# Performance work log

Measured on AMD Instinct MI355X. Metric: run time of the kernel, lower is better.

Reference implementation:

```python
import jax, jax.numpy as jnp
import numpy as np

N_NODES = 100_000
N_EDGES = 3_200_000
D = 64           # node and edge feature dim
HID = 36         # hk.nets.MLP hidden size
OUT = 2          # hk.nets.MLP output size
IN_DIM = 3 * D   # nodes + sent_agg + received_agg (globals are None)


def setup_inputs() -> dict:
    key = jax.random.key(0)
    k_n, k_e, k_s, k_r, k_w1, k_w2 = jax.random.split(key, 6)
    nodes = jax.random.normal(k_n, (N_NODES, D), dtype=jnp.float32)
    edges = jax.random.normal(k_e, (N_EDGES, D), dtype=jnp.float32)
    senders = jax.random.randint(k_s, (N_EDGES,), 0, N_NODES, dtype=jnp.int32)
    receivers = jax.random.randint(k_r, (N_EDGES,), 0, N_NODES, dtype=jnp.int32)
    # haiku Linear default init: truncated normal with stddev 1/sqrt(fan_in); plain normal is fine as a stand-in
    W1 = jax.random.normal(k_w1, (IN_DIM, HID), dtype=jnp.float32) / np.sqrt(IN_DIM)
    b1 = jnp.zeros((HID,), dtype=jnp.float32)
    W2 = jax.random.normal(k_w2, (HID, OUT), dtype=jnp.float32) / np.sqrt(HID)
    b2 = jnp.zeros((OUT,), dtype=jnp.float32)
    return {"nodes": nodes, "edges": edges, "senders": senders,
            "receivers": receivers, "W1": W1, "b1": b1, "W2": W2, "b2": b2}


def reference(nodes, edges, senders, receivers, W1, b1, W2, b2):
    # jraph.GraphNetwork node update with update_edge_fn=None, update_global_fn=None:
    #   sent_attributes     = segment_sum(edges, senders,   num_segments=N)
    #   received_attributes = segment_sum(edges, receivers, num_segments=N)
    #   new_nodes = MLP(concat([nodes, sent, received], axis=-1))
    n = nodes.shape[0]
    sent = jax.ops.segment_sum(edges, senders, num_segments=n)       # [N, D]
    recv = jax.ops.segment_sum(edges, receivers, num_segments=n)     # [N, D]
    feats = jnp.concatenate([nodes, sent, recv], axis=-1)            # [N, 3D]
    h = jax.nn.relu(feats @ W1 + b1)                                 # [N, 36]
    new_nodes = h @ W2 + b2                                          # [N, 2] (activate_final=False)
    return new_nodes
```

## Files before the change

### kernel.cpp

```cpp
#include <hip/hip_runtime.h>
#include <hip/hip_bf16.h>

#define D      64
#define HID    36
#define IN_DIM 192
#define NPB    64
#define MAXNB  2048
#define CHUNK  4096
#define SLICE  64

__global__ void zero_ws_kernel(float4* __restrict__ p, long n4) {
    long i = (long)blockIdx.x * blockDim.x + threadIdx.x;
    long stride = (long)gridDim.x * blockDim.x;
    float4 z = make_float4(0.f, 0.f, 0.f, 0.f);
    for (; i < n4; i += stride) p[i] = z;
}

__global__ __launch_bounds__(256) void scatter_kernel(
    const float* __restrict__ edges,
    const int* __restrict__ senders,
    const int* __restrict__ receivers,
    float* __restrict__ sent,
    float* __restrict__ recv,
    long total)
{
    long i = (long)blockIdx.x * blockDim.x + threadIdx.x;
    if (i >= total) return;
    long e = i >> 6;
    int  d = (int)(i & 63);
    float v = edges[i];
    unsafeAtomicAdd(&sent[(long)senders[e] * D + d], v);
    unsafeAtomicAdd(&recv[(long)receivers[e] * D + d], v);
}

__global__ __launch_bounds__(256) void count_kernel(
    const int* __restrict__ senders,
    const int* __restrict__ receivers,
    int* __restrict__ counts,
    int NB, long E, long total_items)
{
    __shared__ int hist[MAXNB];
    for (int b = threadIdx.x; b < NB; b += 256) hist[b] = 0;
    __syncthreads();

    long start = (long)blockIdx.x * CHUNK;
    long end = start + CHUNK; if (end > total_items) end = total_items;
    for (long i = start + threadIdx.x; i < end; i += 256) {
        int node = (i < E) ? senders[i] : receivers[i - E];
        atomicAdd(&hist[node >> 6], 1);
    }
    __syncthreads();
    int* row = counts + (long)blockIdx.x * NB;
    for (int b = threadIdx.x; b < NB; b += 256) row[b] = hist[b];
}

__global__ __launch_bounds__(256) void colscan1_kernel(
    int* __restrict__ counts, int* __restrict__ psum, int NB, int nblocks)
{
    int b = blockIdx.x * 256 + threadIdx.x;
    if (b >= NB) return;
    int s = blockIdx.y;
    int r0 = s * SLICE;
    int r1 = r0 + SLICE; if (r1 > nblocks) r1 = nblocks;
    int run = 0;
    for (int blk = r0; blk < r1; ++blk) {
        long idx = (long)blk * NB + b;
        int c = counts[idx];
        counts[idx] = run;
        run += c;
    }
    psum[(long)s * NB + b] = run;
}

__global__ __launch_bounds__(256) void colscan2_kernel(
    int* __restrict__ psum, int* __restrict__ tot, int NB, int S)
{
    int b = blockIdx.x * 256 + threadIdx.x;
    if (b >= NB) return;
    int run = 0;
    for (int s = 0; s < S; ++s) {
        long i = (long)s * NB + b;
        int v = psum[i];
        psum[i] = run;
        run += v;
    }
    tot[b] = run;
}

__global__ __launch_bounds__(1024) void basescan_kernel(
    const int* __restrict__ tot, int* __restrict__ base, int NB)
{
    __shared__ int sA[2][MAXNB];
    int t = threadIdx.x;
    sA[0][t]        = (t < NB) ? tot[t] : 0;
    sA[0][t + 1024] = (t + 1024 < NB) ? tot[t + 1024] : 0;
    __syncthreads();
    int src = 0;
    for (int off = 1; off < MAXNB; off <<= 1) {
        int dst = src ^ 1;
        int i0 = t, i1 = t + 1024;
        sA[dst][i0] = sA[src][i0] + ((i0 >= off) ? sA[src][i0 - off] : 0);
        sA[dst][i1] = sA[src][i1] + ((i1 >= off) ? sA[src][i1 - off] : 0);
        src = dst;
        __syncthreads();
    }
    if (t < NB)        base[t]        = (t == 0) ? 0 : sA[src][t - 1];
    if (t + 1024 < NB) base[t + 1024] = sA[src][t + 1023];
}

__global__ __launch_bounds__(256) void scatter_ids_kernel(
    const int* __restrict__ senders,
    const int* __restrict__ receivers,
    const int* __restrict__ counts,
    const int* __restrict__ psum,
    const int* __restrict__ base,
    unsigned* __restrict__ pool,
    int NB, long E, long total_items)
{
    __shared__ int cursor[MAXNB];
    const int* row = counts + (long)blockIdx.x * NB;
    const int* srow = psum + (long)(blockIdx.x / SLICE) * NB;
    for (int b = threadIdx.x; b < NB; b += 256)
        cursor[b] = row[b] + srow[b] + base[b];
    __syncthreads();

    long start = (long)blockIdx.x * CHUNK;
    long end = start + CHUNK; if (end > total_items) end = total_items;
    for (long i = start + threadIdx.x; i < end; i += 256) {
        int dir, node; long edge;
        if (i < E) { dir = 0; edge = i;     node = senders[i]; }
        else       { dir = 1; edge = i - E; node = receivers[i - E]; }
        int b = node >> 6;
        int pos = atomicAdd(&cursor[b], 1);
        pool[pos] = ((unsigned)edge << 7) | ((unsigned)dir << 6) | (unsigned)(node & 63);
    }
}

__global__ __launch_bounds__(256) void sort_bucket_kernel(
    const unsigned* __restrict__ pool,
    const int* __restrict__ base,
    const int* __restrict__ tot,
    unsigned* __restrict__ pool2,
    int4* __restrict__ seg,
    int n_nodes)
{
    __shared__ int hist[4][128];
    __shared__ int cursor[4][128];
    __shared__ int off[128], comb[128], tmp[128];

    int b = blockIdx.x, tid = threadIdx.x;
    int w = tid >> 6, lane = tid & 63;
    int bstart = base[b], cnt = tot[b];

    ((int*)hist)[tid] = 0;
    ((int*)hist)[tid + 256] = 0;
    __syncthreads();

    int q = (cnt + 3) >> 2;
    int rs = w * q;
    int re = rs + q; if (re > cnt) re = cnt;

    for (int i = rs + lane; i < re; i += 64) {
        unsigned r = pool[bstart + i];
        int key = ((r & 63) << 1) | ((r >> 6) & 1);
        atomicAdd(&hist[w][key], 1);
    }
    __syncthreads();

    if (tid < 128) {
        comb[tid] = hist[0][tid] + hist[1][tid] + hist[2][tid] + hist[3][tid];
        tmp[tid] = comb[tid];
    }
    __syncthreads();
    for (int d = 1; d < 128; d <<= 1) {
        int v = 0;
        if (tid < 128) v = (tid >= d) ? tmp[tid - d] : 0;
        __syncthreads();
        if (tid < 128) tmp[tid] += v;
        __syncthreads();
    }
    if (tid < 128) {
        int o = tmp[tid] - comb[tid];
        off[tid] = o;
        int c0 = o + hist[0][tid];
        int c1 = c0 + hist[1][tid];
        int c2 = c1 + hist[2][tid];
        cursor[0][tid] = o;
        cursor[1][tid] = c0;
        cursor[2][tid] = c1;
        cursor[3][tid] = c2;
    }
    __syncthreads();

    if (tid < 64) {
        int node = b * NPB + tid;
        if (node < n_nodes) {
            seg[node] = make_int4(bstart + off[tid * 2],     comb[tid * 2],
                                  bstart + off[tid * 2 + 1], comb[tid * 2 + 1]);
        }
    }

    for (int i = rs + lane; i < re; i += 64) {
        unsigned r = pool[bstart + i];
        int key = ((r & 63) << 1) | ((r >> 6) & 1);
        int pos = atomicAdd(&cursor[w][key], 1);
        pool2[bstart + pos] = r >> 7;
    }
}

__global__ __launch_bounds__(256) void gmlp_kernel(
    const float* __restrict__ edges,
    const unsigned* __restrict__ pool2,
    const int4* __restrict__ seg,
    const float* __restrict__ nodes,
    const float* __restrict__ W1,
    const float* __restrict__ b1,
    const float* __restrict__ W2,
    const float* __restrict__ b2,
    float* __restrict__ out,
    int n_nodes)
{
    __shared__ unsigned sids[4][128];
    __shared__ float sfeat[4][IN_DIM];

    int w = threadIdx.x >> 6, lane = threadIdx.x & 63;
    int node = blockIdx.x * 4 + w;
    if (node >= n_nodes) return;

    int4 si = seg[node];

    float acc2[2];
#pragma unroll
    for (int dir = 0; dir < 2; ++dir) {
        int s = dir ? si.z : si.x;
        int c = dir ? si.w : si.y;
        float acc = 0.f;
        for (int b0 = 0; b0 < c; b0 += 128) {
            int m = c - b0; if (m > 128) m = 128;
            if (lane < m)      sids[w][lane]      = pool2[s + b0 + lane];
            if (64 + lane < m) sids[w][64 + lane] = pool2[s + b0 + 64 + lane];
            int t = 0;
            for (; t + 8 <= m; t += 8) {
                unsigned e0 = sids[w][t],     e1 = sids[w][t + 1];
                unsigned e2 = sids[w][t + 2], e3 = sids[w][t + 3];
                unsigned e4 = sids[w][t + 4], e5 = sids[w][t + 5];
                unsigned e6 = sids[w][t + 6], e7 = sids[w][t + 7];
                float v0 = edges[(long)e0 * D + lane];
                float v1 = edges[(long)e1 * D + lane];
                float v2 = edges[(long)e2 * D + lane];
                float v3 = edges[(long)e3 * D + lane];
                float v4 = edges[(long)e4 * D + lane];
                float v5 = edges[(long)e5 * D + lane];
                float v6 = edges[(long)e6 * D + lane];
                float v7 = edges[(long)e7 * D + lane];
                acc += ((v0 + v1) + (v2 + v3)) + ((v4 + v5) + (v6 + v7));
            }
            for (; t + 4 <= m; t += 4) {
                unsigned e0 = sids[w][t],     e1 = sids[w][t + 1];
                unsigned e2 = sids[w][t + 2], e3 = sids[w][t + 3];
                float v0 = edges[(long)e0 * D + lane];
                float v1 = edges[(long)e1 * D + lane];
                float v2 = edges[(long)e2 * D + lane];
                float v3 = edges[(long)e3 * D + lane];
                acc += (v0 + v1) + (v2 + v3);
            }
            for (; t < m; ++t) acc += edges[(long)sids[w][t] * D + lane];
        }
        acc2[dir] = acc;
    }

    float nf = nodes[(long)node * D + lane];
    sfeat[w][lane]       = nf;
    sfeat[w][64 + lane]  = acc2[0];
    sfeat[w][128 + lane] = acc2[1];

    float h = 0.f;
    if (lane < HID) {
        float h0 = 0.f, h1 = 0.f, h2 = 0.f, h3 = 0.f;
        for (int k = 0; k < IN_DIM; k += 4) {
            h0 += sfeat[w][k]     * W1[(k)     * HID + lane];
            h1 += sfeat[w][k + 1] * W1[(k + 1) * HID + lane];
            h2 += sfeat[w][k + 2] * W1[(k + 2) * HID + lane];
            h3 += sfeat[w][k + 3] * W1[(k + 3) * HID + lane];
        }
        h = fmaxf(b1[lane] + ((h0 + h1) + (h2 + h3)), 0.f);
    }
    float p0 = (lane < HID) ? h * W2[lane * 2 + 0] : 0.f;
    float p1 = (lane < HID) ? h * W2[lane * 2 + 1] : 0.f;
#pragma unroll
    for (int off = 32; off; off >>= 1) {
        p0 += __shfl_down(p0, off, 64);
        p1 += __shfl_down(p1, off, 64);
    }
    if (lane == 0)
        reinterpret_cast<float2*>(out)[node] = make_float2(p0 + b2[0], p1 + b2[1]);
}

__global__ __launch_bounds__(256) void mlp_kernel(
    const float* __restrict__ nodes,
    const float* __restrict__ sent,
    const float* __restrict__ recv,
    const float* __restrict__ W1,
    const float* __restrict__ b1,
    const float* __restrict__ W2,
    const float* __restrict__ b2,
    float* __restrict__ out,
    int n)
{
    __shared__ float sW1[IN_DIM * HID];
    __shared__ float sb1[HID];
    __shared__ float sW2[HID * 2];
    __shared__ float sb2[2];

    for (int t = threadIdx.x; t < IN_DIM * HID; t += blockDim.x) sW1[t] = W1[t];
    if (threadIdx.x < HID)     sb1[threadIdx.x] = b1[threadIdx.x];
    if (threadIdx.x < HID * 2) sW2[threadIdx.x] = W2[threadIdx.x];
    if (threadIdx.x < 2)       sb2[threadIdx.x] = b2[threadIdx.x];
    __syncthreads();

    int node = blockIdx.x * blockDim.x + threadIdx.x;
    if (node >= n) return;

    float acc[HID];
#pragma unroll
    for (int j = 0; j < HID; ++j) acc[j] = sb1[j];

#pragma unroll
    for (int part = 0; part < 3; ++part) {
        const float* f = (part == 0 ? nodes : (part == 1 ? sent : recv)) + (long)node * D;
        const float* wgt = sW1 + part * D * HID;
        for (int k = 0; k < D; k += 4) {
            float4 fv = *reinterpret_cast<const float4*>(f + k);
#pragma unroll
            for (int j = 0; j < HID; ++j) {
                acc[j] += fv.x * wgt[(k + 0) * HID + j];
                acc[j] += fv.y * wgt[(k + 1) * HID + j];
                acc[j] += fv.z * wgt[(k + 2) * HID + j];
                acc[j] += fv.w * wgt[(k + 3) * HID + j];
            }
        }
    }

    float o0 = sb2[0], o1 = sb2[1];
#pragma unroll
    for (int j = 0; j < HID; ++j) {
        float h = fmaxf(acc[j], 0.f);
        o0 += h * sW2[j * 2 + 0];
        o1 += h * sW2[j * 2 + 1];
    }
    reinterpret_cast<float2*>(out)[node] = make_float2(o0, o1);
}

extern "C" void kernel_launch(void* const* d_in, const int* in_sizes, int n_in,
                              void* d_out, int out_size, void* d_ws, size_t ws_size,
                              hipStream_t stream) {
    const float* nodes     = (const float*)d_in[0];
    const float* edges     = (const float*)d_in[1];
    const int*   senders   = (const int*)d_in[2];
    const int*   receivers = (const int*)d_in[3];
    const float* W1        = (const float*)d_in[4];
    const float* b1        = (const float*)d_in[5];
    const float* W2        = (const float*)d_in[6];
    const float* b2        = (const float*)d_in[7];
    float* out = (float*)d_out;

    const int  n_nodes = in_sizes[0] / D;
    const long E       = in_sizes[2];
    const long total_items = 2 * E;

    const int NB      = (n_nodes + NPB - 1) / NPB;
    const int nblocks = (int)((total_items + CHUNK - 1) / CHUNK);
    const int S       = (nblocks + SLICE - 1) / SLICE;

    const size_t sz_sent = (size_t)n_nodes * D * sizeof(float);
    const size_t sz_pool = (size_t)total_items * sizeof(unsigned);
    const size_t sz_seg  = (size_t)n_nodes * sizeof(int4);
    const size_t sz_nb   = (size_t)MAXNB * sizeof(int);
    const size_t sz_psum = (size_t)S * NB * sizeof(int);
    const size_t need    = 2 * sz_sent + 2 * sz_pool + sz_seg + 2 * sz_nb + sz_psum;
    const size_t sz_counts = (size_t)nblocks * NB * sizeof(int);

    char* wp = (char*)d_ws;
    float*    sent  = (float*)wp;           wp += sz_sent;
    float*    recv  = (float*)wp;           wp += sz_sent;
    unsigned* pool  = (unsigned*)wp;        wp += sz_pool;
    unsigned* pool2 = (unsigned*)wp;        wp += sz_pool;
    int4*     seg   = (int4*)wp;            wp += sz_seg;
    int*      tot   = (int*)wp;             wp += sz_nb;
    int*      base  = (int*)wp;             wp += sz_nb;
    int*      psum  = (int*)wp;
    int*      counts = (int*)sent;

    if (ws_size < need || NB > MAXNB || sz_counts > sz_sent) {
        long n4 = (long)n_nodes * D * 2 / 4;
        zero_ws_kernel<<<2048, 256, 0, stream>>>((float4*)d_ws, n4);
        long total = E * D;
        scatter_kernel<<<(int)((total + 255) / 256), 256, 0, stream>>>(
            edges, senders, receivers, sent, recv, total);
        mlp_kernel<<<(n_nodes + 255) / 256, 256, 0, stream>>>(
            nodes, sent, recv, W1, b1, W2, b2, out, n_nodes);
        return;
    }

    count_kernel<<<nblocks, 256, 0, stream>>>(senders, receivers, counts,
                                              NB, E, total_items);
    {
        dim3 g1((NB + 255) / 256, S);
        colscan1_kernel<<<g1, 256, 0, stream>>>(counts, psum, NB, nblocks);
        colscan2_kernel<<<(NB + 255) / 256, 256, 0, stream>>>(psum, tot, NB, S);
    }
    basescan_kernel<<<1, 1024, 0, stream>>>(tot, base, NB);
    scatter_ids_kernel<<<nblocks, 256, 0, stream>>>(senders, receivers, counts,
                                                    psum, base, pool, NB, E, total_items);
    sort_bucket_kernel<<<NB, 256, 0, stream>>>(pool, base, tot, pool2, seg, n_nodes);
    gmlp_kernel<<<(n_nodes + 3) / 4, 256, 0, stream>>>(edges, pool2, seg, nodes,
                                                       W1, b1, W2, b2, out, n_nodes);
}
```

Baseline: 546.6 us.

## Coarsen sort buckets, stage scatter in shared memory, and merge scan kernels

Buckets now hold 256 nodes instead of 64, and each counting/scatter block covers 16384 items instead of 4096. scatter_ids first sorts its chunk's records locally in LDS, then writes them out as contiguous runs per bucket rather than as scattered global writes. The two final scan kernels are merged into one 512-thread kernel, which removes a launch. The cost is larger per-bucket sorts with 512 keys, more LDS per block and lower occupancy, and a new limit of E below 2^23 for the packed edge id, with the old atomic path as fallback.

```diff
diff --git a/kernel.cpp b/kernel.cpp
--- a/kernel.cpp
+++ b/kernel.cpp
@@ -4,9 +4,10 @@
 #define D      64
 #define HID    36
 #define IN_DIM 192
-#define NPB    64
-#define MAXNB  2048
-#define CHUNK  4096
+#define NPB    256
+#define NBMAX  512
+#define KEYS   512
+#define CHUNK  16384
 #define SLICE  64
 
 __global__ void zero_ws_kernel(float4* __restrict__ p, long n4) {
@@ -39,7 +40,7 @@
     int* __restrict__ counts,
     int NB, long E, long total_items)
 {
-    __shared__ int hist[MAXNB];
+    __shared__ int hist[NBMAX];
     for (int b = threadIdx.x; b < NB; b += 256) hist[b] = 0;
     __syncthreads();
 
@@ -47,7 +48,7 @@
     long end = start + CHUNK; if (end > total_items) end = total_items;
     for (long i = start + threadIdx.x; i < end; i += 256) {
         int node = (i < E) ? senders[i] : receivers[i - E];
-        atomicAdd(&hist[node >> 6], 1);
+        atomicAdd(&hist[node >> 8], 1);
     }
     __syncthreads();
     int* row = counts + (long)blockIdx.x * NB;
@@ -72,40 +73,34 @@
     psum[(long)s * NB + b] = run;
 }
 
-__global__ __launch_bounds__(256) void colscan2_kernel(
-    int* __restrict__ psum, int* __restrict__ tot, int NB, int S)
-{
-    int b = blockIdx.x * 256 + threadIdx.x;
-    if (b >= NB) return;
+__global__ __launch_bounds__(512) void colfinish_kernel(
+    int* __restrict__ psum, int* __restrict__ tot, int* __restrict__ base,
+    int NB, int S)
+{
+    __shared__ int sA[2][NBMAX];
+    int t = threadIdx.x;
+
     int run = 0;
-    for (int s = 0; s < S; ++s) {
-        long i = (long)s * NB + b;
-        int v = psum[i];
-        psum[i] = run;
-        run += v;
-    }
-    tot[b] = run;
-}
-
-__global__ __launch_bounds__(1024) void basescan_kernel(
-    const int* __restrict__ tot, int* __restrict__ base, int NB)
-{
-    __shared__ int sA[2][MAXNB];
-    int t = threadIdx.x;
-    sA[0][t]        = (t < NB) ? tot[t] : 0;
-    sA[0][t + 1024] = (t + 1024 < NB) ? tot[t + 1024] : 0;
-    __syncthreads();
+    if (t < NB) {
+        for (int s = 0; s < S; ++s) {
+            long i = (long)s * NB + t;
+            int v = psum[i];
+            psum[i] = run;
+            run += v;
+        }
+        tot[t] = run;
+    }
+    sA[0][t] = (t < NB) ? run : 0;
+    __syncthreads();
+
     int src = 0;
-    for (int off = 1; off < MAXNB; off <<= 1) {
+    for (int off = 1; off < NBMAX; off <<= 1) {
         int dst = src ^ 1;
-        int i0 = t, i1 = t + 1024;
-        sA[dst][i0] = sA[src][i0] + ((i0 >= off) ? sA[src][i0 - off] : 0);
-        sA[dst][i1] = sA[src][i1] + ((i1 >= off) ? sA[src][i1 - off] : 0);
+        sA[dst][t] = sA[src][t] + ((t >= off) ? sA[src][t - off] : 0);
         src = dst;
         __syncthreads();
     }
-    if (t < NB)        base[t]        = (t == 0) ? 0 : sA[src][t - 1];
-    if (t + 1024 < NB) base[t + 1024] = sA[src][t + 1023];
+    if (t < NB) base[t] = (t == 0) ? 0 : sA[src][t - 1];
 }
 
 __global__ __launch_bounds__(256) void scatter_ids_kernel(
@@ -117,22 +112,64 @@
     unsigned* __restrict__ pool,
     int NB, long E, long total_items)
 {
-    __shared__ int cursor[MAXNB];
-    const int* row = counts + (long)blockIdx.x * NB;
-    const int* srow = psum + (long)(blockIdx.x / SLICE) * NB;
-    for (int b = threadIdx.x; b < NB; b += 256)
-        cursor[b] = row[b] + srow[b] + base[b];
+    __shared__ unsigned recs[CHUNK];
+    __shared__ int hist[NBMAX], off[NBMAX], cur[NBMAX], gb[NBMAX], tmp[NBMAX];
+
+    int tid = threadIdx.x;
+    for (int b = tid; b < NBMAX; b += 256) hist[b] = 0;
     __syncthreads();
 
     long start = (long)blockIdx.x * CHUNK;
-    long end = start + CHUNK; if (end > total_items) end = total_items;
-    for (long i = start + threadIdx.x; i < end; i += 256) {
+    long end = start + (long)CHUNK; if (end > total_items) end = total_items;
+    int cnt = (int)(end - start);
+
+    for (int i = tid; i < cnt; i += 256) {
+        long gi = start + i;
+        int node = (gi < E) ? senders[gi] : receivers[gi - E];
+        atomicAdd(&hist[node >> 8], 1);
+    }
+    __syncthreads();
+
+    tmp[tid] = hist[tid];
+    tmp[tid + 256] = hist[tid + 256];
+    __syncthreads();
+    for (int d = 1; d < NBMAX; d <<= 1) {
+        int v0 = (tid >= d) ? tmp[tid - d] : 0;
+        int v1 = (tid + 256 >= d) ? tmp[tid + 256 - d] : 0;
+        __syncthreads();
+        tmp[tid] += v0;
+        tmp[tid + 256] += v1;
+        __syncthreads();
+    }
+    {
+        const int* row  = counts + (long)blockIdx.x * NB;
+        const int* srow = psum + (long)(blockIdx.x / SLICE) * NB;
+        for (int b = tid; b < NBMAX; b += 256) {
+            int o = tmp[b] - hist[b];
+            off[b] = o;
+            cur[b] = o;
+            if (b < NB) gb[b] = row[b] + srow[b] + base[b];
+        }
+    }
+    __syncthreads();
+
+    for (int i = tid; i < cnt; i += 256) {
+        long gi = start + i;
         int dir, node; long edge;
-        if (i < E) { dir = 0; edge = i;     node = senders[i]; }
-        else       { dir = 1; edge = i - E; node = receivers[i - E]; }
-        int b = node >> 6;
-        int pos = atomicAdd(&cursor[b], 1);
-        pool[pos] = ((unsigned)edge << 7) | ((unsigned)dir << 6) | (unsigned)(node & 63);
+        if (gi < E) { dir = 0; edge = gi;     node = senders[gi]; }
+        else        { dir = 1; edge = gi - E; node = receivers[gi - E]; }
+        int b = node >> 8;
+        int pos = atomicAdd(&cur[b], 1);
+        recs[pos] = ((unsigned)edge << 9) | ((unsigned)dir << 8) | (unsigned)(node & 255);
+    }
+    __syncthreads();
+
+    int qw = tid >> 4, ql = tid & 15;
+    for (int b = qw; b < NB; b += 16) {
+        int o = off[b], c = hist[b];
+        long g = gb[b];
+        for (int k = ql; k < c; k += 16)
+            pool[g + k] = recs[o + k];
     }
 }
 
@@ -144,16 +181,15 @@
     int4* __restrict__ seg,
     int n_nodes)
 {
-    __shared__ int hist[4][128];
-    __shared__ int cursor[4][128];
-    __shared__ int off[128], comb[128], tmp[128];
+    __shared__ int hist[4][KEYS];
+    __shared__ int cursor[4][KEYS];
+    __shared__ int off[KEYS], comb[KEYS], tmp[KEYS];
 
     int b = blockIdx.x, tid = threadIdx.x;
     int w = tid >> 6, lane = tid & 63;
     int bstart = base[b], cnt = tot[b];
 
-    ((int*)hist)[tid] = 0;
-    ((int*)hist)[tid + 256] = 0;
+    for (int k = tid; k < 4 * KEYS; k += 256) ((int*)hist)[k] = 0;
     __syncthreads();
 
     int q = (cnt + 3) >> 2;
@@ -162,49 +198,48 @@
 
     for (int i = rs + lane; i < re; i += 64) {
         unsigned r = pool[bstart + i];
-        int key = ((r & 63) << 1) | ((r >> 6) & 1);
+        int key = ((r & 255) << 1) | ((r >> 8) & 1);
         atomicAdd(&hist[w][key], 1);
     }
     __syncthreads();
 
-    if (tid < 128) {
-        comb[tid] = hist[0][tid] + hist[1][tid] + hist[2][tid] + hist[3][tid];
-        tmp[tid] = comb[tid];
-    }
-    __syncthreads();
-    for (int d = 1; d < 128; d <<= 1) {
-        int v = 0;
-        if (tid < 128) v = (tid >= d) ? tmp[tid - d] : 0;
+    comb[tid]       = hist[0][tid] + hist[1][tid] + hist[2][tid] + hist[3][tid];
+    comb[tid + 256] = hist[0][tid + 256] + hist[1][tid + 256]
+                    + hist[2][tid + 256] + hist[3][tid + 256];
+    tmp[tid] = comb[tid];
+    tmp[tid + 256] = comb[tid + 256];
+    __syncthreads();
+    for (int d = 1; d < KEYS; d <<= 1) {
+        int v0 = (tid >= d) ? tmp[tid - d] : 0;
+        int v1 = (tid + 256 >= d) ? tmp[tid + 256 - d] : 0;
         __syncthreads();
-        if (tid < 128) tmp[tid] += v;
+        tmp[tid] += v0;
+        tmp[tid + 256] += v1;
         __syncthreads();
     }
-    if (tid < 128) {
-        int o = tmp[tid] - comb[tid];
-        off[tid] = o;
-        int c0 = o + hist[0][tid];
-        int c1 = c0 + hist[1][tid];
-        int c2 = c1 + hist[2][tid];
-        cursor[0][tid] = o;
-        cursor[1][tid] = c0;
-        cursor[2][tid] = c1;
-        cursor[3][tid] = c2;
-    }
-    __syncthreads();
-
-    if (tid < 64) {
+    for (int k = tid; k < KEYS; k += 256) {
+        int o = tmp[k] - comb[k];
+        off[k] = o;
+        int c0 = o + hist[0][k];
+        int c1 = c0 + hist[1][k];
+        int c2 = c1 + hist[2][k];
+        cursor[0][k] = o;  cursor[1][k] = c0;
+        cursor[2][k] = c1; cursor[3][k] = c2;
+    }
+    __syncthreads();
+
+    {
         int node = b * NPB + tid;
-        if (node < n_nodes) {
+        if (node < n_nodes)
             seg[node] = make_int4(bstart + off[tid * 2],     comb[tid * 2],
                                   bstart + off[tid * 2 + 1], comb[tid * 2 + 1]);
-        }
     }
 
     for (int i = rs + lane; i < re; i += 64) {
         unsigned r = pool[bstart + i];
-        int key = ((r & 63) << 1) | ((r >> 6) & 1);
+        int key = ((r & 255) << 1) | ((r >> 8) & 1);
         int pos = atomicAdd(&cursor[w][key], 1);
-        pool2[bstart + pos] = r >> 7;
+        pool2[bstart + pos] = r >> 9;
     }
 }
 
@@ -375,7 +410,7 @@
     const size_t sz_sent = (size_t)n_nodes * D * sizeof(float);
     const size_t sz_pool = (size_t)total_items * sizeof(unsigned);
     const size_t sz_seg  = (size_t)n_nodes * sizeof(int4);
-    const size_t sz_nb   = (size_t)MAXNB * sizeof(int);
+    const size_t sz_nb   = (size_t)NBMAX * sizeof(int);
     const size_t sz_psum = (size_t)S * NB * sizeof(int);
     const size_t need    = 2 * sz_sent + 2 * sz_pool + sz_seg + 2 * sz_nb + sz_psum;
     const size_t sz_counts = (size_t)nblocks * NB * sizeof(int);
@@ -391,7 +426,7 @@
     int*      psum  = (int*)wp;
     int*      counts = (int*)sent;
 
-    if (ws_size < need || NB > MAXNB || sz_counts > sz_sent) {
+    if (ws_size < need || NB > NBMAX || sz_counts > sz_sent || E >= (1L << 23)) {
         long n4 = (long)n_nodes * D * 2 / 4;
         zero_ws_kernel<<<2048, 256, 0, stream>>>((float4*)d_ws, n4);
         long total = E * D;
@@ -407,9 +442,8 @@
     {
         dim3 g1((NB + 255) / 256, S);
         colscan1_kernel<<<g1, 256, 0, stream>>>(counts, psum, NB, nblocks);
-        colscan2_kernel<<<(NB + 255) / 256, 256, 0, stream>>>(psum, tot, NB, S);
-    }
-    basescan_kernel<<<1, 1024, 0, stream>>>(tot, base, NB);
+        colfinish_kernel<<<1, 512, 0, stream>>>(psum, tot, base, NB, S);
+    }
     scatter_ids_kernel<<<nblocks, 256, 0, stream>>>(senders, receivers, counts,
                                                     psum, base, pool, NB, E, total_items);
     sort_bucket_kernel<<<NB, 256, 0, stream>>>(pool, base, tot, pool2, seg, n_nodes);
```

New measurement: 539.7 us. No clear change (-1.3%).
